# Kernel optimization log

Hardware: AMD Instinct MI355X
Metric: run time of the kernel (lower is better)

## Reference

```python
import jax, jax.numpy as jnp
import numpy as np

B, S, D, H = 4, 2048, 1024, 16
HD = D // H  # head_dim = 64


def setup_inputs() -> dict:
    key = jax.random.key(0)
    k1, k2, k3 = jax.random.split(key, 3)
    x = jax.random.normal(k1, (B, S, D), dtype=jnp.float32)
    # causal mask, broadcast over batch and heads
    mask = jnp.tril(jnp.ones((S, S), dtype=jnp.int32))[None, None, :, :]
    Wqkv = jax.random.normal(k2, (D, 3 * D), dtype=jnp.float32) * (1.0 / np.sqrt(D))
    bqkv = jnp.zeros((3 * D,), dtype=jnp.float32)
    Wout = jax.random.normal(k3, (D, D), dtype=jnp.float32) * (1.0 / np.sqrt(D))
    bout = jnp.zeros((D,), dtype=jnp.float32)
    return {"x": x, "mask": mask, "Wqkv": Wqkv, "bqkv": bqkv, "Wout": Wout, "bout": bout}


def reference(x, mask, Wqkv, bqkv, Wout, bout):
    b, s, _ = x.shape
    qkv = x @ Wqkv + bqkv                       # [b, s, 3D]
    q, k, v = jnp.split(qkv, 3, axis=-1)
    # [b, s, D] -> [b, H, s, HD]
    def to_heads(t):
        return t.reshape(b, s, H, HD).transpose(0, 2, 1, 3)
    q, k, v = to_heads(q), to_heads(k), to_heads(v)
    scores = jnp.einsum("bhqd,bhkd->bhqk", q, k) / jnp.sqrt(jnp.float32(HD))
    scores = jnp.where(mask == 0, jnp.float32(-1e9), scores)
    attn = jax.nn.softmax(scores, axis=-1)      # dropout is identity in eval
    ctx = jnp.einsum("bhqk,bhkd->bhqd", attn, v)
    ctx = ctx.transpose(0, 2, 1, 3).reshape(b, s, D)
    return ctx @ Wout + bout
```

## Files before the change

### kernel.cpp

```cpp
#include <hip/hip_runtime.h>

typedef __bf16 bf16_t;
typedef __bf16 bf16x4_t __attribute__((ext_vector_type(4)));
typedef __bf16 bf16x8_t __attribute__((ext_vector_type(8)));
typedef float  f32x4_t  __attribute__((ext_vector_type(4)));
typedef unsigned int u32x4_t __attribute__((ext_vector_type(4)));
typedef unsigned short u16;

#define MFMA_BF16(a, b, c) __builtin_amdgcn_mfma_f32_16x16x32_bf16((a), (b), (c), 0, 0, 0)

typedef __attribute__((address_space(1))) const unsigned int gu32_t;
typedef __attribute__((address_space(3))) unsigned int su32_t;
static __device__ __forceinline__ void gload_lds16(const void* g, void* l) {
  __builtin_amdgcn_global_load_lds((gu32_t*)g, (su32_t*)l, 16, 0, 0);
}

static __device__ __forceinline__ f32x4_t zero4() {
  f32x4_t z; z[0] = 0.f; z[1] = 0.f; z[2] = 0.f; z[3] = 0.f; return z;
}
static __device__ __forceinline__ bf16x8_t load8(const void* p) {
  return __builtin_bit_cast(bf16x8_t, *reinterpret_cast<const u32x4_t*>(p));
}

constexpr int BB = 4, SS = 2048, DD = 1024, HH = 16, HDD = 64;
constexpr int MR = BB * SS;
constexpr int NQKV = 3 * DD;

__global__ __launch_bounds__(256, 2) void k_convert_x(const float* __restrict__ x,
                                                      bf16_t* __restrict__ xb) {
  int i = blockIdx.x * 256 + threadIdx.x;
  f32x4_t v = reinterpret_cast<const f32x4_t*>(x)[i];
  bf16x4_t o;
  o[0] = (bf16_t)v[0]; o[1] = (bf16_t)v[1]; o[2] = (bf16_t)v[2]; o[3] = (bf16_t)v[3];
  reinterpret_cast<bf16x4_t*>(xb)[i] = o;
}

template <int KD, int ND>
__global__ __launch_bounds__(256, 2) void k_transpose(const float* __restrict__ W,
                                                      bf16_t* __restrict__ WT) {
  __shared__ float tile[64][65];
  const int nt = ND / 64;
  int bx = blockIdx.x % nt;
  int by = blockIdx.x / nt;
  int k0 = by * 64, n0 = bx * 64;
  int t = threadIdx.x, cc = t & 63;
#pragma unroll
  for (int i = 0; i < 16; ++i) {
    int rr = (t >> 6) + i * 4;
    tile[rr][cc] = W[(k0 + rr) * ND + n0 + cc];
  }
  __syncthreads();
#pragma unroll
  for (int i = 0; i < 16; ++i) {
    int rr = (t >> 6) + i * 4;
    WT[(n0 + rr) * (long)KD + k0 + cc] = (bf16_t)tile[cc][rr];
  }
}

__device__ __forceinline__ void gemm_core_128(const bf16_t* __restrict__ A,
                                              const bf16_t* __restrict__ BT,
                                              int m0, int n0,
                                              u16* As, u16* Bs, f32x4_t acc[4][4]) {
  const int tid = threadIdx.x;
  const int w = tid >> 6, l = tid & 63;
  const int g = l >> 4, li = l & 15;
  const int wm = w >> 1, wn = w & 1;
  const int srow = tid >> 3;
  const int sch = (tid & 7) ^ (srow & 7);
#pragma unroll
  for (int i = 0; i < 4; ++i)
#pragma unroll
    for (int j = 0; j < 4; ++j) acc[i][j] = zero4();

  for (int kt = 0; kt < 16; ++kt) {
    const int k0 = kt * 64;
    const bf16_t* ga = A  + (long)(m0 + srow) * 1024 + k0 + sch * 8;
    const bf16_t* gb = BT + (long)(n0 + srow) * 1024 + k0 + sch * 8;
    char* la = (char*)As + w * 1024;
    char* lb = (char*)Bs + w * 1024;
#pragma unroll
    for (int i = 0; i < 4; ++i) {
      gload_lds16(ga + (long)i * 32 * 1024, la + i * 4096);
      gload_lds16(gb + (long)i * 32 * 1024, lb + i * 4096);
    }
    __syncthreads();
#pragma unroll
    for (int kk = 0; kk < 2; ++kk) {
      const int c0 = ((kk * 4 + g) ^ (li & 7)) * 8;
      bf16x8_t af[4], bfr[4];
#pragma unroll
      for (int f = 0; f < 4; ++f) {
        af[f]  = load8(&As[(wm * 64 + f * 16 + li) * 64 + c0]);
        bfr[f] = load8(&Bs[(wn * 64 + f * 16 + li) * 64 + c0]);
      }
#pragma unroll
      for (int fm = 0; fm < 4; ++fm)
#pragma unroll
        for (int fn = 0; fn < 4; ++fn)
          acc[fm][fn] = MFMA_BF16(af[fm], bfr[fn], acc[fm][fn]);
    }
    __syncthreads();
  }
}

__global__ __launch_bounds__(256, 2) void k_gemm_qkv(const bf16_t* __restrict__ xb,
                                                     const bf16_t* __restrict__ WqkvT,
                                                     const float* __restrict__ bqkv,
                                                     bf16_t* __restrict__ qb,
                                                     bf16_t* __restrict__ kb,
                                                     bf16_t* __restrict__ vtb) {
  __shared__ u16 As[128 * 64];
  __shared__ u16 Bs[128 * 64];
  f32x4_t acc[4][4];
  int nb = blockIdx.x;
  int bid = (nb & 7) * 192 + (nb >> 3);
  int tn = bid % 24, tm = bid / 24;
  int m0 = tm * 128, n0 = tn * 128;
  gemm_core_128(xb, WqkvT, m0, n0, As, Bs, acc);

  const int tid = threadIdx.x, w = tid >> 6, l = tid & 63, g = l >> 4, li = l & 15;
  const int wm = w >> 1, wn = w & 1;
  const int which = n0 >> 10;
#pragma unroll
  for (int fm = 0; fm < 4; ++fm) {
#pragma unroll
    for (int fn = 0; fn < 4; ++fn) {
      int n = n0 + wn * 64 + fn * 16 + li;
      float bias = bqkv[n];
      int d = n & 1023, h = d >> 6, hd = d & 63;
      int mbase = m0 + wm * 64 + fm * 16 + g * 4;
      int b = mbase >> 11, s = mbase & 2047;
      int bh = b * HH + h;
      if (which == 0) {
#pragma unroll
        for (int r = 0; r < 4; ++r) {
          float v = (acc[fm][fn][r] + bias) * 0.125f;
          qb[((long)bh * SS + s + r) * HDD + hd] = (bf16_t)v;
        }
      } else if (which == 1) {
#pragma unroll
        for (int r = 0; r < 4; ++r)
          kb[((long)bh * SS + s + r) * HDD + hd] = (bf16_t)(acc[fm][fn][r] + bias);
      } else {
        bf16x4_t pv;
#pragma unroll
        for (int r = 0; r < 4; ++r) pv[r] = (bf16_t)(acc[fm][fn][r] + bias);
        *reinterpret_cast<bf16x4_t*>(&vtb[((long)bh * HDD + hd) * SS + s]) = pv;
      }
    }
  }
}

__global__ __launch_bounds__(256, 4) void k_attn(const bf16_t* __restrict__ qb,
                                                 const bf16_t* __restrict__ kb,
                                                 const bf16_t* __restrict__ vtb,
                                                 bf16_t* __restrict__ ctx) {
  __shared__ u16 Ks[2][64 * 64];
  __shared__ u16 Vs[2][64 * 64];
  __shared__ u16 Plds[4][16 * 64];
  int nb = blockIdx.x;
  int bid = (nb & 7) * 256 + (nb >> 3);
  int bh = bid >> 5, qt = bid & 31;
  int tid = threadIdx.x, w = tid >> 6, l = tid & 63, g = l >> 4, li = l & 15;
  int q0 = qt * 64;
  const int srow = tid >> 3;
  const int sch = (tid & 7) ^ (srow & 7);

  const bf16_t* qrow = qb + ((long)bh * SS + q0 + w * 16 + li) * HDD;
  bf16x8_t qa[2];
  qa[0] = load8(qrow + g * 8);
  qa[1] = load8(qrow + 32 + g * 8);

  const bf16_t* Kg = kb + (long)bh * SS * HDD;
  const bf16_t* Vg = vtb + (long)bh * HDD * SS;
  u16* Pw = &Plds[w][0];

  float mrow[4], lrow[4];
  f32x4_t acc[4];
#pragma unroll
  for (int r = 0; r < 4; ++r) { mrow[r] = -1e30f; lrow[r] = 0.f; }
#pragma unroll
  for (int fd = 0; fd < 4; ++fd) acc[fd] = zero4();

  {
    char* lk = (char*)&Ks[0][0] + w * 1024;
    char* lv = (char*)&Vs[0][0] + w * 1024;
#pragma unroll
    for (int i = 0; i < 2; ++i) {
      gload_lds16(Kg + (long)(i * 32 + srow) * HDD + sch * 8, lk + i * 4096);
      gload_lds16(Vg + (long)(i * 32 + srow) * SS + sch * 8, lv + i * 4096);
    }
  }
  __syncthreads();

  int buf = 0;
  for (int j = 0; j <= qt; ++j) {
    if (j < qt) {
      int k0n = (j + 1) * 64;
      char* lk = (char*)&Ks[buf ^ 1][0] + w * 1024;
      char* lv = (char*)&Vs[buf ^ 1][0] + w * 1024;
#pragma unroll
      for (int i = 0; i < 2; ++i) {
        gload_lds16(Kg + (long)(k0n + i * 32 + srow) * HDD + sch * 8, lk + i * 4096);
        gload_lds16(Vg + (long)(i * 32 + srow) * SS + k0n + sch * 8, lv + i * 4096);
      }
    }
    const u16* Ksb = &Ks[buf][0];
    const u16* Vsb = &Vs[buf][0];
    f32x4_t sf[4];
    __builtin_amdgcn_s_setprio(1);
#pragma unroll
    for (int fc = 0; fc < 4; ++fc) {
      sf[fc] = zero4();
#pragma unroll
      for (int ds = 0; ds < 2; ++ds) {
        bf16x8_t kf = load8(&Ksb[(fc * 16 + li) * 64 + ((ds * 4 + g) ^ (li & 7)) * 8]);
        sf[fc] = MFMA_BF16(qa[ds], kf, sf[fc]);
      }
    }
    __builtin_amdgcn_s_setprio(0);
    if (j == qt) {
#pragma unroll
      for (int fc = 0; fc < 4; ++fc)
#pragma unroll
        for (int r = 0; r < 4; ++r) {
          int col = fc * 16 + li, row = w * 16 + g * 4 + r;
          if (col > row) sf[fc][r] = -1e30f;
        }
    }
    float sc[4];
#pragma unroll
    for (int r = 0; r < 4; ++r) {
      float pm = fmaxf(fmaxf(sf[0][r], sf[1][r]), fmaxf(sf[2][r], sf[3][r]));
#pragma unroll
      for (int off = 8; off; off >>= 1) pm = fmaxf(pm, __shfl_xor(pm, off));
      float mnew = fmaxf(mrow[r], pm);
      sc[r] = __expf(mrow[r] - mnew);
      mrow[r] = mnew;
    }
    float rs[4];
#pragma unroll
    for (int r = 0; r < 4; ++r) rs[r] = 0.f;
#pragma unroll
    for (int fc = 0; fc < 4; ++fc)
#pragma unroll
      for (int r = 0; r < 4; ++r) {
        float p = __expf(sf[fc][r] - mrow[r]);
        sf[fc][r] = p;
        rs[r] += p;
      }
#pragma unroll
    for (int r = 0; r < 4; ++r) {
#pragma unroll
      for (int off = 8; off; off >>= 1) rs[r] += __shfl_xor(rs[r], off);
      lrow[r] = lrow[r] * sc[r] + rs[r];
    }
#pragma unroll
    for (int fd = 0; fd < 4; ++fd)
#pragma unroll
      for (int r = 0; r < 4; ++r) acc[fd][r] *= sc[r];
#pragma unroll
    for (int fc = 0; fc < 4; ++fc)
#pragma unroll
      for (int r = 0; r < 4; ++r) {
        int prow = g * 4 + r;
        int c = (fc * 2 + (li >> 3)) ^ (prow & 7);
        Pw[prow * 64 + c * 8 + (li & 7)] = __builtin_bit_cast(u16, (bf16_t)sf[fc][r]);
      }
    __builtin_amdgcn_s_setprio(1);
#pragma unroll
    for (int ss = 0; ss < 2; ++ss) {
      bf16x8_t pa = load8(&Pw[li * 64 + (((ss * 4 + g) ^ (li & 7)) * 8)]);
#pragma unroll
      for (int fd = 0; fd < 4; ++fd) {
        bf16x8_t vf = load8(&Vsb[(fd * 16 + li) * 64 + ((ss * 4 + g) ^ (li & 7)) * 8]);
        acc[fd] = MFMA_BF16(pa, vf, acc[fd]);
      }
    }
    __builtin_amdgcn_s_setprio(0);
    __syncthreads();
    buf ^= 1;
  }
  int b = bh >> 4, h = bh & 15;
#pragma unroll
  for (int fd = 0; fd < 4; ++fd)
#pragma unroll
    for (int r = 0; r < 4; ++r) {
      int srw = q0 + w * 16 + g * 4 + r;
      float v = acc[fd][r] / lrow[r];
      ctx[((long)b * SS + srw) * DD + h * HDD + fd * 16 + li] = (bf16_t)v;
    }
}

__global__ __launch_bounds__(256, 2) void k_gemm_out(const bf16_t* __restrict__ ctx,
                                                     const bf16_t* __restrict__ WoutT,
                                                     const float* __restrict__ bout,
                                                     float* __restrict__ out) {
  __shared__ u16 As[128 * 64];
  __shared__ u16 Bs[128 * 64];
  f32x4_t acc[4][4];
  int nb = blockIdx.x;
  int bid = (nb & 7) * 64 + (nb >> 3);
  int tn = bid & 7, tm = bid >> 3;
  int m0 = tm * 128, n0 = tn * 128;
  gemm_core_128(ctx, WoutT, m0, n0, As, Bs, acc);

  const int tid = threadIdx.x, w = tid >> 6, l = tid & 63, g = l >> 4, li = l & 15;
  const int wm = w >> 1, wn = w & 1;
#pragma unroll
  for (int fm = 0; fm < 4; ++fm)
#pragma unroll
    for (int fn = 0; fn < 4; ++fn) {
      int n = n0 + wn * 64 + fn * 16 + li;
      float bias = bout[n];
      int m = m0 + wm * 64 + fm * 16 + g * 4;
#pragma unroll
      for (int r = 0; r < 4; ++r)
        out[(long)(m + r) * DD + n] = acc[fm][fn][r] + bias;
    }
}

extern "C" void kernel_launch(void* const* d_in, const int* in_sizes, int n_in,
                              void* d_out, int out_size, void* d_ws, size_t ws_size,
                              hipStream_t stream) {
  const float* x    = (const float*)d_in[0];
  const float* Wqkv = (const float*)d_in[2];
  const float* bqkv = (const float*)d_in[3];
  const float* Wout = (const float*)d_in[4];
  const float* bout = (const float*)d_in[5];
  float* out = (float*)d_out;

  char* ws = (char*)d_ws;
  bf16_t* WqkvT = (bf16_t*)ws;
  bf16_t* WoutT = (bf16_t*)(ws + 6291456);
  bf16_t* qb    = (bf16_t*)(ws + 6291456 + 2097152);
  bf16_t* kb    = qb + (long)MR * DD;
  bf16_t* vtb   = kb + (long)MR * DD;
  bf16_t* xb    = vtb + (long)MR * DD;
  bf16_t* ctx   = xb;

  k_convert_x<<<MR * DD / 1024, 256, 0, stream>>>(x, xb);
  k_transpose<1024, 3072><<<(3072 / 64) * (1024 / 64), 256, 0, stream>>>(Wqkv, WqkvT);
  k_transpose<1024, 1024><<<(1024 / 64) * (1024 / 64), 256, 0, stream>>>(Wout, WoutT);
  k_gemm_qkv<<<(MR / 128) * (NQKV / 128), 256, 0, stream>>>(xb, WqkvT, bqkv, qb, kb, vtb);
  k_attn<<<BB * HH * (SS / 64), 256, 0, stream>>>(qb, kb, vtb, ctx);
  k_gemm_out<<<(MR / 128) * (DD / 128), 256, 0, stream>>>(ctx, WoutT, bout, out);
}
```

Measured before the change: 321.8 us.

## Compute transposed scores so softmax stats are per-lane; skip rescale when max unchanged

Swaps the MFMA operand order so each lane holds one query row's scores across keys. Row max and sum now need only two cross-lane shuffles instead of four per row, and each lane keeps a single running max and sum. The accumulator rescale is skipped when no row max grew anywhere in the wave. The P write to LDS is reindexed to match the transposed layout, which may change LDS write bank patterns, and the rescale now needs broadcast shuffles.

```diff
diff --git a/kernel.cpp b/kernel.cpp
--- a/kernel.cpp
+++ b/kernel.cpp
@@ -175,10 +175,8 @@
   const bf16_t* Vg = vtb + (long)bh * HDD * SS;
   u16* Pw = &Plds[w][0];
 
-  float mrow[4], lrow[4];
+  float m_s = -1e30f, l_s = 0.f;
   f32x4_t acc[4];
-#pragma unroll
-  for (int r = 0; r < 4; ++r) { mrow[r] = -1e30f; lrow[r] = 0.f; }
 #pragma unroll
   for (int fd = 0; fd < 4; ++fd) acc[fd] = zero4();
 
@@ -207,15 +205,15 @@
     }
     const u16* Ksb = &Ks[buf][0];
     const u16* Vsb = &Vs[buf][0];
-    f32x4_t sf[4];
+    f32x4_t sfT[4];
     __builtin_amdgcn_s_setprio(1);
 #pragma unroll
     for (int fc = 0; fc < 4; ++fc) {
-      sf[fc] = zero4();
+      sfT[fc] = zero4();
 #pragma unroll
       for (int ds = 0; ds < 2; ++ds) {
         bf16x8_t kf = load8(&Ksb[(fc * 16 + li) * 64 + ((ds * 4 + g) ^ (li & 7)) * 8]);
-        sf[fc] = MFMA_BF16(qa[ds], kf, sf[fc]);
+        sfT[fc] = MFMA_BF16(kf, qa[ds], sfT[fc]);
       }
     }
     __builtin_amdgcn_s_setprio(0);
@@ -224,48 +222,49 @@
       for (int fc = 0; fc < 4; ++fc)
 #pragma unroll
         for (int r = 0; r < 4; ++r) {
-          int col = fc * 16 + li, row = w * 16 + g * 4 + r;
-          if (col > row) sf[fc][r] = -1e30f;
+          int kk = fc * 16 + g * 4 + r, qq = w * 16 + li;
+          if (kk > qq) sfT[fc][r] = -1e30f;
         }
     }
-    float sc[4];
-#pragma unroll
-    for (int r = 0; r < 4; ++r) {
-      float pm = fmaxf(fmaxf(sf[0][r], sf[1][r]), fmaxf(sf[2][r], sf[3][r]));
-#pragma unroll
-      for (int off = 8; off; off >>= 1) pm = fmaxf(pm, __shfl_xor(pm, off));
-      float mnew = fmaxf(mrow[r], pm);
-      sc[r] = __expf(mrow[r] - mnew);
-      mrow[r] = mnew;
-    }
-    float rs[4];
-#pragma unroll
-    for (int r = 0; r < 4; ++r) rs[r] = 0.f;
+    float pm01 = fmaxf(fmaxf(sfT[0][0], sfT[0][1]), fmaxf(sfT[0][2], sfT[0][3]));
+    float pm23 = fmaxf(fmaxf(sfT[1][0], sfT[1][1]), fmaxf(sfT[1][2], sfT[1][3]));
+    float pm45 = fmaxf(fmaxf(sfT[2][0], sfT[2][1]), fmaxf(sfT[2][2], sfT[2][3]));
+    float pm67 = fmaxf(fmaxf(sfT[3][0], sfT[3][1]), fmaxf(sfT[3][2], sfT[3][3]));
+    float pm = fmaxf(fmaxf(pm01, pm23), fmaxf(pm45, pm67));
+    pm = fmaxf(pm, __shfl_xor(pm, 16));
+    pm = fmaxf(pm, __shfl_xor(pm, 32));
+    bool noresc = __all(pm <= m_s);
+    float mnew = fmaxf(m_s, pm);
+    float scale = __expf(m_s - mnew);
+    m_s = mnew;
+    float rs = 0.f;
 #pragma unroll
     for (int fc = 0; fc < 4; ++fc)
 #pragma unroll
       for (int r = 0; r < 4; ++r) {
-        float p = __expf(sf[fc][r] - mrow[r]);
-        sf[fc][r] = p;
-        rs[r] += p;
-      }
-#pragma unroll
-    for (int r = 0; r < 4; ++r) {
-#pragma unroll
-      for (int off = 8; off; off >>= 1) rs[r] += __shfl_xor(rs[r], off);
-      lrow[r] = lrow[r] * sc[r] + rs[r];
-    }
-#pragma unroll
-    for (int fd = 0; fd < 4; ++fd)
-#pragma unroll
-      for (int r = 0; r < 4; ++r) acc[fd][r] *= sc[r];
+        float p = __expf(sfT[fc][r] - mnew);
+        sfT[fc][r] = p;
+        rs += p;
+      }
+    rs += __shfl_xor(rs, 16);
+    rs += __shfl_xor(rs, 32);
+    l_s = l_s * scale + rs;
+    if (!noresc) {
+      float scb[4];
+#pragma unroll
+      for (int r = 0; r < 4; ++r) scb[r] = __shfl(scale, g * 4 + r);
+#pragma unroll
+      for (int fd = 0; fd < 4; ++fd)
+#pragma unroll
+        for (int r = 0; r < 4; ++r) acc[fd][r] *= scb[r];
+    }
 #pragma unroll
     for (int fc = 0; fc < 4; ++fc)
 #pragma unroll
       for (int r = 0; r < 4; ++r) {
-        int prow = g * 4 + r;
-        int c = (fc * 2 + (li >> 3)) ^ (prow & 7);
-        Pw[prow * 64 + c * 8 + (li & 7)] = __builtin_bit_cast(u16, (bf16_t)sf[fc][r]);
+        int kk = fc * 16 + g * 4 + r;
+        Pw[li * 64 + (((kk >> 3) ^ (li & 7)) * 8) + (kk & 7)] =
+            __builtin_bit_cast(u16, (bf16_t)sfT[fc][r]);
       }
     __builtin_amdgcn_s_setprio(1);
 #pragma unroll
@@ -281,13 +280,16 @@
     __syncthreads();
     buf ^= 1;
   }
+  float lb[4];
+#pragma unroll
+  for (int r = 0; r < 4; ++r) lb[r] = __shfl(l_s, g * 4 + r);
   int b = bh >> 4, h = bh & 15;
 #pragma unroll
   for (int fd = 0; fd < 4; ++fd)
 #pragma unroll
     for (int r = 0; r < 4; ++r) {
       int srw = q0 + w * 16 + g * 4 + r;
-      float v = acc[fd][r] / lrow[r];
+      float v = acc[fd][r] / lb[r];
       ctx[((long)b * SS + srw) * DD + h * HDD + fd * 16 + li] = (bf16_t)v;
     }
 }
```

Result: faster. 301.5 us (-6.3%).
